# Kernel tuning notes

Measured on AMD Instinct MI355X. Metric: run time of the kernel, lower is better.

## Reference

```python
import jax, jax.numpy as jnp
import numpy as np

B, S, A, M = 8, 64, 9, 64          # batch, feature-map side, anchors/pos, max gt boxes
IMG_H, IMG_W = 800.0, 800.0
MATCH_IOU = 0.5                     # match_iou_threshold from __init__


def setup_inputs() -> dict:
    key = jax.random.key(0)
    k1, k2, k3, k4 = jax.random.split(key, 4)
    rpn_bbox_offset_pred = jax.random.normal(k1, (B, S, S, A, 4), jnp.float32) * 0.1
    # second-stage (fast rcnn) offsets for every proposal
    fast_rcnn_offsets = jax.random.normal(k2, (B, S * S * A, 4), jnp.float32) * 0.1
    # valid padded gt boxes in corner format (x1,y1,x2,y2)
    xy = jax.random.uniform(k3, (B, M, 2), jnp.float32, 0.0, 600.0)
    wh = jax.random.uniform(k4, (B, M, 2), jnp.float32, 10.0, 200.0)
    gt_bbox = jnp.concatenate([xy, jnp.minimum(xy + wh, 800.0)], axis=-1)
    # standard 3 scales x 3 ratios anchors
    scales = jnp.array([64.0, 128.0, 256.0], jnp.float32)
    ratios = jnp.array([0.5, 1.0, 2.0], jnp.float32)
    anchor_heights = (scales[:, None] * jnp.sqrt(ratios)[None, :]).reshape(-1)
    anchor_widths = (scales[:, None] / jnp.sqrt(ratios)[None, :]).reshape(-1)
    return dict(rpn_bbox_offset_pred=rpn_bbox_offset_pred,
                fast_rcnn_offsets=fast_rcnn_offsets,
                gt_bbox=gt_bbox,
                anchor_heights=anchor_heights,
                anchor_widths=anchor_widths)


def _decode_rpn(offsets, anchor_h, anchor_w):
    """convert_rpn_bbox_offsets_to_rpn_bbox: anchor-relative offsets -> corner boxes.
    offsets: (B,S,S,A,4) -> (B, S*S*A, 4) clipped to the image."""
    stride_y, stride_x = IMG_H / S, IMG_W / S
    acy = ((jnp.arange(S, dtype=jnp.float32) + 0.5) * stride_y)[:, None, None]  # (S,1,1)
    acx = ((jnp.arange(S, dtype=jnp.float32) + 0.5) * stride_x)[None, :, None]  # (1,S,1)
    ah = anchor_h[None, None, :]  # (1,1,A)
    aw = anchor_w[None, None, :]
    tx, ty, tw, th = offsets[..., 0], offsets[..., 1], offsets[..., 2], offsets[..., 3]
    pcx = acx + tx * aw
    pcy = acy + ty * ah
    pw = aw * jnp.exp(tw)
    ph = ah * jnp.exp(th)
    x1 = jnp.clip(pcx - 0.5 * pw, 0.0, IMG_W)
    y1 = jnp.clip(pcy - 0.5 * ph, 0.0, IMG_H)
    x2 = jnp.clip(pcx + 0.5 * pw, 0.0, IMG_W)
    y2 = jnp.clip(pcy + 0.5 * ph, 0.0, IMG_H)
    return jnp.stack([x1, y1, x2, y2], axis=-1).reshape(offsets.shape[0], -1, 4)


def _box_iou(a, b):
    """torchvision.ops.box_iou: a (N,4), b (M,4) -> (N,M)."""
    area_a = (a[:, 2] - a[:, 0]) * (a[:, 3] - a[:, 1])
    area_b = (b[:, 2] - b[:, 0]) * (b[:, 3] - b[:, 1])
    lt = jnp.maximum(a[:, None, :2], b[None, :, :2])  # (N,M,2)
    rb = jnp.minimum(a[:, None, 2:], b[None, :, 2:])
    wh = jnp.clip(rb - lt, 0.0)
    inter = wh[..., 0] * wh[..., 1]
    return inter / (area_a[:, None] + area_b[None, :] - inter + 1e-9)


def _apply_offsets(boxes, off):
    """apply_offsets_to_fast_rcnn_bbox, exactly as in the torch module."""
    w = boxes[..., 2] - boxes[..., 0]
    h = boxes[..., 3] - boxes[..., 1]
    x1 = off[..., 0] * w + boxes[..., 0]
    y1 = off[..., 1] * h + boxes[..., 1]
    x2 = x1 + jnp.exp(off[..., 2]) * w
    y2 = y1 + jnp.exp(off[..., 3]) * h
    return jnp.stack([x1, y1, x2, y2], axis=-1)


def reference(rpn_bbox_offset_pred, fast_rcnn_offsets, gt_bbox, anchor_heights, anchor_widths):
    # 1. bbox offset decode (anchors -> proposals)
    rpn_bbox_pred = _decode_rpn(rpn_bbox_offset_pred, anchor_heights, anchor_widths)  # (B,N,4)
    # 2. per-image box_iou matching (vectorized over the batch)
    ious = jax.vmap(_box_iou)(rpn_bbox_pred, gt_bbox)  # (B,N,M)
    best_iou = jnp.max(ious, axis=-1)                  # (B,N)
    best_gt_index = jnp.argmax(ious, axis=-1)          # (B,N) int
    is_foreground = best_iou > MATCH_IOU               # rpn_objectness_gt
    # 3. second-stage offset decode on the proposals
    refined_bbox = _apply_offsets(rpn_bbox_pred, fast_rcnn_offsets)  # (B,N,4)
    return rpn_bbox_pred, is_foreground, best_gt_index, refined_bbox
```

## Files before the change

### kernel.cpp

```cpp
#include <hip/hip_runtime.h>

#define BB 8
#define SS 64
#define AA 9
#define MM 64
#define NN (SS * SS * AA)

__global__ __launch_bounds__(256) void frcnn_head_kernel(
    const float* __restrict__ rpn_off,
    const float* __restrict__ frc_off,
    const float* __restrict__ gt,
    const float* __restrict__ anchor_h,
    const float* __restrict__ anchor_w,
    float* __restrict__ out)
{
    __shared__ float gt_s[MM * 4];
    __shared__ float area_s[MM];
    __shared__ float ah_s[AA];
    __shared__ float aw_s[AA];

    const int blocks_per_b = NN / 256;
    const int b     = blockIdx.x / blocks_per_b;
    const int chunk = blockIdx.x % blocks_per_b;
    const int tid   = threadIdx.x;
    const int i     = chunk * 256 + tid;

    if (tid < MM * 4) gt_s[tid] = gt[(size_t)b * MM * 4 + tid];
    if (tid < AA) { ah_s[tid] = anchor_h[tid]; aw_s[tid] = anchor_w[tid]; }
    __syncthreads();
    if (tid < MM) {
        const float gx1 = gt_s[tid * 4 + 0], gy1 = gt_s[tid * 4 + 1];
        const float gx2 = gt_s[tid * 4 + 2], gy2 = gt_s[tid * 4 + 3];
        area_s[tid] = (gx2 - gx1) * (gy2 - gy1);
    }
    __syncthreads();

    const int a_idx = i % AA;
    const int xy    = i / AA;
    const int gx    = xy % SS;
    const int gy    = xy / SS;
    const float stride = 800.0f / (float)SS;
    const float acx = ((float)gx + 0.5f) * stride;
    const float acy = ((float)gy + 0.5f) * stride;

    const float4 t = ((const float4*)rpn_off)[(size_t)b * NN + i];
    const float aw = aw_s[a_idx];
    const float ah = ah_s[a_idx];

    const float pcx = acx + t.x * aw;
    const float pcy = acy + t.y * ah;
    const float pw  = aw * expf(t.z);
    const float ph  = ah * expf(t.w);

    const float bx1 = fminf(fmaxf(pcx - 0.5f * pw, 0.0f), 800.0f);
    const float by1 = fminf(fmaxf(pcy - 0.5f * ph, 0.0f), 800.0f);
    const float bx2 = fminf(fmaxf(pcx + 0.5f * pw, 0.0f), 800.0f);
    const float by2 = fminf(fmaxf(pcy + 0.5f * ph, 0.0f), 800.0f);

    const float area = (bx2 - bx1) * (by2 - by1);
    float best  = -1.0f;
    int   bestj = 0;
    #pragma unroll 8
    for (int j = 0; j < MM; ++j) {
        const float gx1 = gt_s[j * 4 + 0], gy1 = gt_s[j * 4 + 1];
        const float gx2 = gt_s[j * 4 + 2], gy2 = gt_s[j * 4 + 3];
        const float ix1 = fmaxf(bx1, gx1);
        const float iy1 = fmaxf(by1, gy1);
        const float ix2 = fminf(bx2, gx2);
        const float iy2 = fminf(by2, gy2);
        const float iw = fmaxf(ix2 - ix1, 0.0f);
        const float ih = fmaxf(iy2 - iy1, 0.0f);
        const float inter = iw * ih;
        const float iou = inter / (area + area_s[j] - inter + 1e-9f);
        if (iou > best) { best = iou; bestj = j; }
    }

    const float4 f = ((const float4*)frc_off)[(size_t)b * NN + i];
    const float w = bx2 - bx1;
    const float h = by2 - by1;
    const float rx1 = f.x * w + bx1;
    const float ry1 = f.y * h + by1;
    const float rx2 = rx1 + expf(f.z) * w;
    const float ry2 = ry1 + expf(f.w) * h;

    const size_t BN  = (size_t)BB * NN;
    const size_t o1  = BN * 4;
    const size_t o2  = o1 + BN;
    const size_t o3  = o2 + BN;
    const size_t idx = (size_t)b * NN + i;

    ((float4*)out)[idx] = make_float4(bx1, by1, bx2, by2);
    out[o1 + idx] = (best > 0.5f) ? 1.0f : 0.0f;
    out[o2 + idx] = (float)bestj;
    ((float4*)(out + o3))[idx] = make_float4(rx1, ry1, rx2, ry2);
}

extern "C" void kernel_launch(void* const* d_in, const int* in_sizes, int n_in,
                              void* d_out, int out_size, void* d_ws, size_t ws_size,
                              hipStream_t stream) {
    const float* rpn_off  = (const float*)d_in[0];
    const float* frc_off  = (const float*)d_in[1];
    const float* gt       = (const float*)d_in[2];
    const float* anchor_h = (const float*)d_in[3];
    const float* anchor_w = (const float*)d_in[4];
    float* out = (float*)d_out;

    const int grid = BB * (NN / 256);
    frcnn_head_kernel<<<grid, 256, 0, stream>>>(rpn_off, frc_off, gt,
                                                anchor_h, anchor_w, out);
}
```

Baseline: 23.44 us.

## Process two anchors per thread and replace IoU division with cross-multiplied compare

Each thread now handles two proposals, so every shared-memory read of a gt box and its area is reused across two IoU evaluations. The per-iteration division is replaced by tracking the best numerator and denominator and comparing by cross-multiplication, with the threshold test also done without dividing. The grid is halved. The cross-multiplied compare can break ties or near-ties differently from a true division. Fewer blocks also means less parallelism.

```diff
diff --git a/kernel.cpp b/kernel.cpp
--- a/kernel.cpp
+++ b/kernel.cpp
@@ -19,11 +19,12 @@
     __shared__ float ah_s[AA];
     __shared__ float aw_s[AA];
 
-    const int blocks_per_b = NN / 256;
+    const int blocks_per_b = NN / 512;
     const int b     = blockIdx.x / blocks_per_b;
     const int chunk = blockIdx.x % blocks_per_b;
     const int tid   = threadIdx.x;
-    const int i     = chunk * 256 + tid;
+    const int i0    = chunk * 512 + tid;
+    const int i1    = i0 + 256;
 
     if (tid < MM * 4) gt_s[tid] = gt[(size_t)b * MM * 4 + tid];
     if (tid < AA) { ah_s[tid] = anchor_h[tid]; aw_s[tid] = anchor_w[tid]; }
@@ -35,64 +36,82 @@
     }
     __syncthreads();
 
-    const int a_idx = i % AA;
-    const int xy    = i / AA;
-    const int gx    = xy % SS;
-    const int gy    = xy / SS;
     const float stride = 800.0f / (float)SS;
-    const float acx = ((float)gx + 0.5f) * stride;
-    const float acy = ((float)gy + 0.5f) * stride;
+    float bx1[2], by1[2], bx2[2], by2[2], area[2];
+    const int ii[2] = { i0, i1 };
+    #pragma unroll
+    for (int k = 0; k < 2; ++k) {
+        const int i     = ii[k];
+        const int a_idx = i % AA;
+        const int xy    = i / AA;
+        const int gx    = xy % SS;
+        const int gy    = xy / SS;
+        const float acx = ((float)gx + 0.5f) * stride;
+        const float acy = ((float)gy + 0.5f) * stride;
 
-    const float4 t = ((const float4*)rpn_off)[(size_t)b * NN + i];
-    const float aw = aw_s[a_idx];
-    const float ah = ah_s[a_idx];
+        const float4 t = ((const float4*)rpn_off)[(size_t)b * NN + i];
+        const float aw = aw_s[a_idx];
+        const float ah = ah_s[a_idx];
 
-    const float pcx = acx + t.x * aw;
-    const float pcy = acy + t.y * ah;
-    const float pw  = aw * expf(t.z);
-    const float ph  = ah * expf(t.w);
+        const float pcx = acx + t.x * aw;
+        const float pcy = acy + t.y * ah;
+        const float pw  = aw * expf(t.z);
+        const float ph  = ah * expf(t.w);
 
-    const float bx1 = fminf(fmaxf(pcx - 0.5f * pw, 0.0f), 800.0f);
-    const float by1 = fminf(fmaxf(pcy - 0.5f * ph, 0.0f), 800.0f);
-    const float bx2 = fminf(fmaxf(pcx + 0.5f * pw, 0.0f), 800.0f);
-    const float by2 = fminf(fmaxf(pcy + 0.5f * ph, 0.0f), 800.0f);
+        bx1[k] = fminf(fmaxf(pcx - 0.5f * pw, 0.0f), 800.0f);
+        by1[k] = fminf(fmaxf(pcy - 0.5f * ph, 0.0f), 800.0f);
+        bx2[k] = fminf(fmaxf(pcx + 0.5f * pw, 0.0f), 800.0f);
+        by2[k] = fminf(fmaxf(pcy + 0.5f * ph, 0.0f), 800.0f);
+        area[k] = (bx2[k] - bx1[k]) * (by2[k] - by1[k]);
+    }
 
-    const float area = (bx2 - bx1) * (by2 - by1);
-    float best  = -1.0f;
-    int   bestj = 0;
-    #pragma unroll 8
+    float bnum[2] = { -1.0f, -1.0f };
+    float bden[2] = {  1.0f,  1.0f };
+    int   bj[2]   = {  0, 0 };
+    #pragma unroll 4
     for (int j = 0; j < MM; ++j) {
         const float gx1 = gt_s[j * 4 + 0], gy1 = gt_s[j * 4 + 1];
         const float gx2 = gt_s[j * 4 + 2], gy2 = gt_s[j * 4 + 3];
-        const float ix1 = fmaxf(bx1, gx1);
-        const float iy1 = fmaxf(by1, gy1);
-        const float ix2 = fminf(bx2, gx2);
-        const float iy2 = fminf(by2, gy2);
-        const float iw = fmaxf(ix2 - ix1, 0.0f);
-        const float ih = fmaxf(iy2 - iy1, 0.0f);
-        const float inter = iw * ih;
-        const float iou = inter / (area + area_s[j] - inter + 1e-9f);
-        if (iou > best) { best = iou; bestj = j; }
+        const float ga  = area_s[j];
+        #pragma unroll
+        for (int k = 0; k < 2; ++k) {
+            const float ix1 = fmaxf(bx1[k], gx1);
+            const float iy1 = fmaxf(by1[k], gy1);
+            const float ix2 = fminf(bx2[k], gx2);
+            const float iy2 = fminf(by2[k], gy2);
+            const float iw  = fmaxf(ix2 - ix1, 0.0f);
+            const float ih  = fmaxf(iy2 - iy1, 0.0f);
+            const float inter = iw * ih;
+            const float den   = area[k] + ga - inter + 1e-9f;
+            if (inter * bden[k] > bnum[k] * den) {
+                bnum[k] = inter; bden[k] = den; bj[k] = j;
+            }
+        }
     }
 
-    const float4 f = ((const float4*)frc_off)[(size_t)b * NN + i];
-    const float w = bx2 - bx1;
-    const float h = by2 - by1;
-    const float rx1 = f.x * w + bx1;
-    const float ry1 = f.y * h + by1;
-    const float rx2 = rx1 + expf(f.z) * w;
-    const float ry2 = ry1 + expf(f.w) * h;
+    const size_t BN = (size_t)BB * NN;
+    const size_t o1 = BN * 4;
+    const size_t o2 = o1 + BN;
+    const size_t o3 = o2 + BN;
 
-    const size_t BN  = (size_t)BB * NN;
-    const size_t o1  = BN * 4;
-    const size_t o2  = o1 + BN;
-    const size_t o3  = o2 + BN;
-    const size_t idx = (size_t)b * NN + i;
+    #pragma unroll
+    for (int k = 0; k < 2; ++k) {
+        const int i = ii[k];
+        const size_t idx = (size_t)b * NN + i;
 
-    ((float4*)out)[idx] = make_float4(bx1, by1, bx2, by2);
-    out[o1 + idx] = (best > 0.5f) ? 1.0f : 0.0f;
-    out[o2 + idx] = (float)bestj;
-    ((float4*)(out + o3))[idx] = make_float4(rx1, ry1, rx2, ry2);
+        const float4 f = ((const float4*)frc_off)[(size_t)b * NN + i];
+        const float w = bx2[k] - bx1[k];
+        const float h = by2[k] - by1[k];
+        const float rx1 = f.x * w + bx1[k];
+        const float ry1 = f.y * h + by1[k];
+        const float rx2 = rx1 + expf(f.z) * w;
+        const float ry2 = ry1 + expf(f.w) * h;
+
+        ((float4*)out)[idx] = make_float4(bx1[k], by1[k], bx2[k], by2[k]);
+        out[o1 + idx] = (bnum[k] > 0.5f * bden[k]) ? 1.0f : 0.0f;
+        out[o2 + idx] = (float)bj[k];
+        ((float4*)(out + o3))[idx] = make_float4(rx1, ry1, rx2, ry2);
+    }
 }
 
 extern "C" void kernel_launch(void* const* d_in, const int* in_sizes, int n_in,
@@ -105,7 +124,7 @@
     const float* anchor_w = (const float*)d_in[4];
     float* out = (float*)d_out;
 
-    const int grid = BB * (NN / 256);
+    const int grid = BB * (NN / 512);
     frcnn_head_kernel<<<grid, 256, 0, stream>>>(rpn_off, frc_off, gt,
                                                 anchor_h, anchor_w, out);
 }
```

Result: faster. 20.93 us (-10.7%).
